# Optimization experiments

Hardware: AMD Instinct MI355X
Metric: run time of the kernel (lower is better)

Reference implementation:

```python
import jax, jax.numpy as jnp
import numpy as np

B, S, D = 2, 2048, 1024
H = 16
HD = D // H
MINUS_INFINITY = -1000000000.0


def setup_inputs() -> dict:
    key = jax.random.key(0)
    ks = jax.random.split(key, 6)
    sc = 0.02
    return {
        "x": jax.random.normal(ks[0], (B, S, D), dtype=jnp.float32),
        "Wq": jax.random.normal(ks[1], (D, D), dtype=jnp.float32) * sc,
        "Wk": jax.random.normal(ks[2], (D, D), dtype=jnp.float32) * sc,
        "Wv": jax.random.normal(ks[3], (D, D), dtype=jnp.float32) * sc,
        "Wo": jax.random.normal(ks[4], (D, D), dtype=jnp.float32) * sc,
        "bo": jnp.zeros((D,), dtype=jnp.float32),
    }


def reference(x, Wq, Wk, Wv, Wo, bo):
    b, n, _ = x.shape
    # Linear with transpose_b=True: x @ W.T
    q = jnp.einsum('bnd,ed->bne', x, Wq).reshape(b, n, H, HD).transpose(0, 2, 1, 3)
    k = jnp.einsum('bnd,ed->bne', x, Wk).reshape(b, n, H, HD).transpose(0, 2, 1, 3)
    v = jnp.einsum('bnd,ed->bne', x, Wv).reshape(b, n, H, HD).transpose(0, 2, 1, 3)
    scores = jnp.einsum('bhqd,bhkd->bhqk', q, k) * (1.0 / HD ** 0.5)
    mask = jnp.triu(jnp.ones((n, n), dtype=scores.dtype), k=1) * MINUS_INFINITY
    scores = scores + mask[None, None, :, :]
    attn = jax.nn.softmax(scores, axis=-1)  # dropout prob = 0.0
    ctx = jnp.einsum('bhqk,bhkd->bhqd', attn, v)
    ctx = ctx.transpose(0, 2, 1, 3).reshape(b, n, D)
    return jnp.einsum('bnd,ed->bne', ctx, Wo) + bo
```

## Files before the change

### kernel.cpp

```cpp
#include <hip/hip_runtime.h>
#include <hip/hip_bf16.h>

#define B_  2
#define S_  2048
#define D_  1024
#define H_  16
#define HD_ 64

typedef __attribute__((ext_vector_type(8))) short short8;
typedef __attribute__((ext_vector_type(4))) float f32x4;

__device__ __forceinline__ unsigned short f2b(float f) {
    __hip_bfloat16 h = __float2bfloat16(f);
    unsigned short u;
    __builtin_memcpy(&u, &h, 2);
    return u;
}

typedef __attribute__((address_space(1))) const unsigned int g_u32;
typedef __attribute__((address_space(3))) unsigned int l_u32;
__device__ __forceinline__ void gload_lds16(const void* g, void* l) {
    __builtin_amdgcn_global_load_lds((g_u32*)g, (l_u32*)l, 16, 0, 0);
}

__global__ __launch_bounds__(256) void convert_kernel(
    const float* __restrict__ x,  const float* __restrict__ Wq,
    const float* __restrict__ Wk, const float* __restrict__ Wv,
    const float* __restrict__ Wo, unsigned short* __restrict__ dst)
{
    const long long i4 = blockIdx.x * 256 + threadIdx.x;
    const long long e  = i4 * 4;
    const long long M1 = 1048576LL;
    const float* src;
    if      (e < 4 * M1) src = x  + e;
    else if (e < 5 * M1) src = Wq + (e - 4 * M1);
    else if (e < 6 * M1) src = Wk + (e - 5 * M1);
    else if (e < 7 * M1) src = Wv + (e - 6 * M1);
    else                 src = Wo + (e - 7 * M1);
    float4 v = *(const float4*)src;
    unsigned long long pk = (unsigned long long)f2b(v.x)
                          | ((unsigned long long)f2b(v.y) << 16)
                          | ((unsigned long long)f2b(v.z) << 32)
                          | ((unsigned long long)f2b(v.w) << 48);
    *(unsigned long long*)&dst[e] = pk;
}

__global__ __launch_bounds__(256) void qkv_proj_kernel(
    const unsigned short* __restrict__ x,
    const unsigned short* __restrict__ Wq,
    const unsigned short* __restrict__ Wk,
    const unsigned short* __restrict__ Wv,
    unsigned short* __restrict__ q_ws,
    unsigned short* __restrict__ k_ws,
    unsigned short* __restrict__ vT_ws)
{
    __shared__ unsigned short a_lds[128 * 64];
    __shared__ unsigned short b_lds[128 * 64];

    const int m0 = blockIdx.x * 128;
    const int n0 = blockIdx.y * 128;
    const int which = blockIdx.z;
    const unsigned short* W = (which == 0) ? Wq : (which == 1) ? Wk : Wv;

    const int tid  = threadIdx.x;
    const int wave = tid >> 6;
    const int lane = tid & 63;
    const int l15  = lane & 15;
    const int quad = lane >> 4;
    const int wm = (wave & 1) * 64;
    const int wn = (wave >> 1) * 64;
    const int xr = (l15 & 7) << 3;

    f32x4 acc[4][4];
    #pragma unroll
    for (int sm = 0; sm < 4; ++sm)
        #pragma unroll
        for (int sn = 0; sn < 4; ++sn)
            #pragma unroll
            for (int r = 0; r < 4; ++r) acc[sm][sn][r] = 0.f;

    for (int kk = 0; kk < D_; kk += 64) {
        #pragma unroll
        for (int p = 0; p < 4; ++p) {
            const int off = (p * 256 + tid) * 16;
            const int r   = off >> 7;
            const int cs  = ((off & 127) >> 1) ^ ((r & 7) << 3);
            gload_lds16(&x[(m0 + r) * D_ + kk + cs], &a_lds[off >> 1]);
            gload_lds16(&W[(n0 + r) * D_ + kk + cs], &b_lds[off >> 1]);
        }
        __syncthreads();
        #pragma unroll
        for (int kc = 0; kc < 2; ++kc) {
            const int cswz = (kc * 32 + quad * 8) ^ xr;
            short8 af[4], bf[4];
            #pragma unroll
            for (int s = 0; s < 4; ++s) {
                af[s] = *(const short8*)&a_lds[(wm + s * 16 + l15) * 64 + cswz];
                bf[s] = *(const short8*)&b_lds[(wn + s * 16 + l15) * 64 + cswz];
            }
            #pragma unroll
            for (int sm = 0; sm < 4; ++sm)
                #pragma unroll
                for (int sn = 0; sn < 4; ++sn)
                    acc[sm][sn] = __builtin_amdgcn_mfma_f32_16x16x32_bf16(
                        af[sm], bf[sn], acc[sm][sn], 0, 0, 0);
        }
        __syncthreads();
    }

    #pragma unroll
    for (int sm = 0; sm < 4; ++sm) {
        #pragma unroll
        for (int sn = 0; sn < 4; ++sn) {
            const int n  = n0 + wn + sn * 16 + l15;
            const int h  = n >> 6;
            const int hd = n & 63;
            const int mbase = m0 + wm + sm * 16 + quad * 4;
            const int b     = mbase >> 11;
            const int sbase = mbase & 2047;
            if (which == 2) {
                unsigned long long pk = 0;
                #pragma unroll
                for (int r = 0; r < 4; ++r)
                    pk |= (unsigned long long)f2b(acc[sm][sn][r]) << (16 * r);
                *(unsigned long long*)&vT_ws[((b * H_ + h) * HD_ + hd) * S_ + sbase] = pk;
            } else if (which == 0) {
                #pragma unroll
                for (int r = 0; r < 4; ++r)
                    q_ws[((b * H_ + h) * S_ + (sbase + r)) * HD_ + hd] =
                        f2b(acc[sm][sn][r] * 0.125f);
            } else {
                #pragma unroll
                for (int r = 0; r < 4; ++r)
                    k_ws[((b * H_ + h) * S_ + (sbase + r)) * HD_ + hd] =
                        f2b(acc[sm][sn][r]);
            }
        }
    }
}

__global__ __launch_bounds__(256) void attn_kernel(
    const unsigned short* __restrict__ q_ws,
    const unsigned short* __restrict__ k_ws,
    const unsigned short* __restrict__ vT_ws,
    unsigned short* __restrict__ ctx_ws)
{
    __shared__ unsigned short k_lds[2][64][72];
    __shared__ unsigned short vT_lds[2][64][72];

    const int bh = blockIdx.x;
    const int qt = 31 - (int)blockIdx.y;

    const int tid  = threadIdx.x;
    const int wave = tid >> 6;
    const int lane = tid & 63;
    const int l15  = lane & 15;
    const int quad = lane >> 4;
    const int row  = tid >> 3;
    const int c8   = tid & 7;

    const unsigned short* Qh = q_ws + bh * (S_ * HD_);
    const unsigned short* Kh = k_ws + bh * (S_ * HD_);
    const unsigned short* Vt = vT_ws + bh * (HD_ * S_);
    const int b = bh >> 4;
    const int h = bh & 15;

    const int src0 = l15 + 32 * (quad & 1);
    const int src1 = src0 + 16;
    const int sel  = quad >> 1;

    const int q0 = qt * 64;
    const int qg = q0 + wave * 16 + l15;

    *(uint4*)&k_lds[0][row][c8 * 8]       = *(const uint4*)&Kh[row * HD_ + c8 * 8];
    *(uint4*)&k_lds[0][row + 32][c8 * 8]  = *(const uint4*)&Kh[(row + 32) * HD_ + c8 * 8];
    *(uint4*)&vT_lds[0][row][c8 * 8]      = *(const uint4*)&Vt[row * S_ + c8 * 8];
    *(uint4*)&vT_lds[0][row + 32][c8 * 8] = *(const uint4*)&Vt[(row + 32) * S_ + c8 * 8];

    short8 aq[2];
    aq[0] = *(const short8*)&Qh[qg * HD_ + quad * 8];
    aq[1] = *(const short8*)&Qh[qg * HD_ + 32 + quad * 8];

    __syncthreads();

    float l_lane = 0.f;
    f32x4 o[4];
    #pragma unroll
    for (int f = 0; f < 4; ++f)
        #pragma unroll
        for (int r = 0; r < 4; ++r) o[f][r] = 0.f;

    for (int kt = 0; kt <= qt; ++kt) {
        const int cur = kt & 1;
        if (kt < qt) {
            const int nk0 = (kt + 1) * 64;
            const int nb  = cur ^ 1;
            *(uint4*)&k_lds[nb][row][c8 * 8]       = *(const uint4*)&Kh[(nk0 + row) * HD_ + c8 * 8];
            *(uint4*)&k_lds[nb][row + 32][c8 * 8]  = *(const uint4*)&Kh[(nk0 + row + 32) * HD_ + c8 * 8];
            *(uint4*)&vT_lds[nb][row][c8 * 8]      = *(const uint4*)&Vt[row * S_ + nk0 + c8 * 8];
            *(uint4*)&vT_lds[nb][row + 32][c8 * 8] = *(const uint4*)&Vt[(row + 32) * S_ + nk0 + c8 * 8];
        }

        f32x4 sc[4];
        #pragma unroll
        for (int f = 0; f < 4; ++f)
            #pragma unroll
            for (int r = 0; r < 4; ++r) sc[f][r] = 0.f;
        #pragma unroll
        for (int f = 0; f < 4; ++f)
            #pragma unroll
            for (int kc = 0; kc < 2; ++kc) {
                short8 ak = *(const short8*)&k_lds[cur][f * 16 + l15][kc * 32 + quad * 8];
                sc[f] = __builtin_amdgcn_mfma_f32_16x16x32_bf16(ak, aq[kc], sc[f], 0, 0, 0);
            }

        float p[4][4];
        if (kt == qt) {
            const int kbase = kt * 64 + quad * 4;
            #pragma unroll
            for (int f = 0; f < 4; ++f)
                #pragma unroll
                for (int r = 0; r < 4; ++r) {
                    const float pv = __expf(sc[f][r]);
                    p[f][r] = (kbase + f * 16 + r > qg) ? 0.f : pv;
                    l_lane += p[f][r];
                }
        } else {
            #pragma unroll
            for (int f = 0; f < 4; ++f)
                #pragma unroll
                for (int r = 0; r < 4; ++r) {
                    p[f][r] = __expf(sc[f][r]);
                    l_lane += p[f][r];
                }
        }

        unsigned int pd[4][2];
        #pragma unroll
        for (int f = 0; f < 4; ++f) {
            pd[f][0] = (unsigned int)f2b(p[f][0]) | ((unsigned int)f2b(p[f][1]) << 16);
            pd[f][1] = (unsigned int)f2b(p[f][2]) | ((unsigned int)f2b(p[f][3]) << 16);
        }

        #pragma unroll
        for (int c = 0; c < 2; ++c) {
            const int a0 = __shfl((int)pd[c * 2][0],     src0, 64);
            const int a1 = __shfl((int)pd[c * 2][1],     src0, 64);
            const int a2 = __shfl((int)pd[c * 2][0],     src1, 64);
            const int a3 = __shfl((int)pd[c * 2][1],     src1, 64);
            const int b0 = __shfl((int)pd[c * 2 + 1][0], src0, 64);
            const int b1 = __shfl((int)pd[c * 2 + 1][1], src0, 64);
            const int b2 = __shfl((int)pd[c * 2 + 1][0], src1, 64);
            const int b3 = __shfl((int)pd[c * 2 + 1][1], src1, 64);
            union { int i[4]; short8 s; } u2;
            u2.i[0] = sel ? b0 : a0;
            u2.i[1] = sel ? b1 : a1;
            u2.i[2] = sel ? b2 : a2;
            u2.i[3] = sel ? b3 : a3;
            #pragma unroll
            for (int f = 0; f < 4; ++f) {
                short8 av = *(const short8*)&vT_lds[cur][f * 16 + l15][c * 32 + quad * 8];
                o[f] = __builtin_amdgcn_mfma_f32_16x16x32_bf16(av, u2.s, o[f], 0, 0, 0);
            }
        }

        __syncthreads();
    }

    float l = l_lane;
    l += __shfl_xor(l, 16, 64);
    l += __shfl_xor(l, 32, 64);
    const float inv_l = 1.0f / l;

    #pragma unroll
    for (int f = 0; f < 4; ++f) {
        unsigned long long pk = 0;
        #pragma unroll
        for (int r = 0; r < 4; ++r)
            pk |= (unsigned long long)f2b(o[f][r] * inv_l) << (16 * r);
        *(unsigned long long*)&ctx_ws[(b * S_ + qg) * D_ + h * 64 + f * 16 + quad * 4] = pk;
    }
}

__global__ __launch_bounds__(256) void out_proj_kernel(
    const unsigned short* __restrict__ ctx,
    const unsigned short* __restrict__ Wo,
    const float* __restrict__ bo,
    float* __restrict__ out)
{
    __shared__ unsigned short a_lds[128 * 64];
    __shared__ unsigned short b_lds[128 * 64];

    const int m0 = blockIdx.x * 128;
    const int n0 = blockIdx.y * 128;

    const int tid  = threadIdx.x;
    const int wave = tid >> 6;
    const int lane = tid & 63;
    const int l15  = lane & 15;
    const int quad = lane >> 4;
    const int wm = (wave & 1) * 64;
    const int wn = (wave >> 1) * 64;
    const int xr = (l15 & 7) << 3;

    f32x4 acc[4][4];
    #pragma unroll
    for (int sm = 0; sm < 4; ++sm)
        #pragma unroll
        for (int sn = 0; sn < 4; ++sn)
            #pragma unroll
            for (int r = 0; r < 4; ++r) acc[sm][sn][r] = 0.f;

    for (int kk = 0; kk < D_; kk += 64) {
        #pragma unroll
        for (int p = 0; p < 4; ++p) {
            const int off = (p * 256 + tid) * 16;
            const int r   = off >> 7;
            const int cs  = ((off & 127) >> 1) ^ ((r & 7) << 3);
            gload_lds16(&ctx[(m0 + r) * D_ + kk + cs], &a_lds[off >> 1]);
            gload_lds16(&Wo[(n0 + r) * D_ + kk + cs],  &b_lds[off >> 1]);
        }
        __syncthreads();
        #pragma unroll
        for (int kc = 0; kc < 2; ++kc) {
            const int cswz = (kc * 32 + quad * 8) ^ xr;
            short8 af[4], bf[4];
            #pragma unroll
            for (int s = 0; s < 4; ++s) {
                af[s] = *(const short8*)&a_lds[(wm + s * 16 + l15) * 64 + cswz];
                bf[s] = *(const short8*)&b_lds[(wn + s * 16 + l15) * 64 + cswz];
            }
            #pragma unroll
            for (int sm = 0; sm < 4; ++sm)
                #pragma unroll
                for (int sn = 0; sn < 4; ++sn)
                    acc[sm][sn] = __builtin_amdgcn_mfma_f32_16x16x32_bf16(
                        af[sm], bf[sn], acc[sm][sn], 0, 0, 0);
        }
        __syncthreads();
    }

    #pragma unroll
    for (int sm = 0; sm < 4; ++sm) {
        #pragma unroll
        for (int sn = 0; sn < 4; ++sn) {
            const int n = n0 + wn + sn * 16 + l15;
            const float bias = bo[n];
            const int mbase = m0 + wm + sm * 16 + quad * 4;
            #pragma unroll
            for (int r = 0; r < 4; ++r)
                out[(mbase + r) * D_ + n] = acc[sm][sn][r] + bias;
        }
    }
}

extern "C" void kernel_launch(void* const* d_in, const int* in_sizes, int n_in,
                              void* d_out, int out_size, void* d_ws, size_t ws_size,
                              hipStream_t stream) {
    const float* x  = (const float*)d_in[0];
    const float* Wq = (const float*)d_in[1];
    const float* Wk = (const float*)d_in[2];
    const float* Wv = (const float*)d_in[3];
    const float* Wo = (const float*)d_in[4];
    const float* bo = (const float*)d_in[5];
    float* out = (float*)d_out;

    const size_t M1 = 1048576;
    const size_t SZ = 4 * M1;

    unsigned short* xb  = (unsigned short*)d_ws;
    unsigned short* wqb = xb  + SZ;
    unsigned short* wkb = wqb + M1;
    unsigned short* wvb = wkb + M1;
    unsigned short* wob = wvb + M1;
    unsigned short* q_ws   = wob + M1;
    unsigned short* k_ws   = q_ws + SZ;
    unsigned short* vT_ws  = k_ws + SZ;
    unsigned short* ctx_ws = vT_ws + SZ;

    convert_kernel<<<dim3(8192), 256, 0, stream>>>(x, Wq, Wk, Wv, Wo, xb);
    qkv_proj_kernel<<<dim3(32, 8, 3), 256, 0, stream>>>(xb, wqb, wkb, wvb, q_ws, k_ws, vT_ws);
    attn_kernel<<<dim3(32, 32), 256, 0, stream>>>(q_ws, k_ws, vT_ws, ctx_ws);
    out_proj_kernel<<<dim3(32, 8), 256, 0, stream>>>(ctx_ws, wob, bo, out);
}
```

Measured before the change: 182.1 us.

## Load attention K/V tiles directly to LDS with XOR swizzle and exp2 softmax

The attention kernel now stages K and V^T tiles with global_load_lds (direct global-to-LDS) instead of going through registers. It replaces the padded LDS layout with an unpadded one that uses an XOR swizzle to avoid bank conflicts. Q is pre-scaled by log2(e) so the softmax can use exp2 instead of exp, and s_setprio raises wave priority around the MFMA blocks. This is meant to cut register traffic and VALU work in the inner loop. The direct LDS loads depend on the existing barrier for correctness with double buffering.

Result: no change. 185.4 us (+1.8%).

```diff
diff --git a/kernel.cpp b/kernel.cpp
--- a/kernel.cpp
+++ b/kernel.cpp
@@ -128,7 +128,7 @@
                 #pragma unroll
                 for (int r = 0; r < 4; ++r)
                     q_ws[((b * H_ + h) * S_ + (sbase + r)) * HD_ + hd] =
-                        f2b(acc[sm][sn][r] * 0.125f);
+                        f2b(acc[sm][sn][r] * (0.125f * 1.44269504f));
             } else {
                 #pragma unroll
                 for (int r = 0; r < 4; ++r)
@@ -145,8 +145,8 @@
     const unsigned short* __restrict__ vT_ws,
     unsigned short* __restrict__ ctx_ws)
 {
-    __shared__ unsigned short k_lds[2][64][72];
-    __shared__ unsigned short vT_lds[2][64][72];
+    __shared__ unsigned short k_lds[2 * 64 * 64];
+    __shared__ unsigned short vT_lds[2 * 64 * 64];
 
     const int bh = blockIdx.x;
     const int qt = 31 - (int)blockIdx.y;
@@ -156,7 +156,7 @@
     const int lane = tid & 63;
     const int l15  = lane & 15;
     const int quad = lane >> 4;
-    const int row  = tid >> 3;
+    const int r0   = tid >> 3;
     const int c8   = tid & 7;
 
     const unsigned short* Qh = q_ws + bh * (S_ * HD_);
@@ -169,13 +169,17 @@
     const int src1 = src0 + 16;
     const int sel  = quad >> 1;
 
-    const int q0 = qt * 64;
-    const int qg = q0 + wave * 16 + l15;
-
-    *(uint4*)&k_lds[0][row][c8 * 8]       = *(const uint4*)&Kh[row * HD_ + c8 * 8];
-    *(uint4*)&k_lds[0][row + 32][c8 * 8]  = *(const uint4*)&Kh[(row + 32) * HD_ + c8 * 8];
-    *(uint4*)&vT_lds[0][row][c8 * 8]      = *(const uint4*)&Vt[row * S_ + c8 * 8];
-    *(uint4*)&vT_lds[0][row + 32][c8 * 8] = *(const uint4*)&Vt[(row + 32) * S_ + c8 * 8];
+    const int qg = qt * 64 + wave * 16 + l15;
+
+    const int scol = (c8 ^ (r0 & 7)) * 8;
+    const int d0 = r0 * 64 + c8 * 8;
+    const int d1 = d0 + 2048;
+    const int xr8 = (l15 & 7) << 3;
+
+    gload_lds16(&Kh[r0 * HD_ + scol],        &k_lds[d0]);
+    gload_lds16(&Kh[(r0 + 32) * HD_ + scol], &k_lds[d1]);
+    gload_lds16(&Vt[r0 * S_ + scol],         &vT_lds[d0]);
+    gload_lds16(&Vt[(r0 + 32) * S_ + scol],  &vT_lds[d1]);
 
     short8 aq[2];
     aq[0] = *(const short8*)&Qh[qg * HD_ + quad * 8];
@@ -191,14 +195,14 @@
         for (int r = 0; r < 4; ++r) o[f][r] = 0.f;
 
     for (int kt = 0; kt <= qt; ++kt) {
-        const int cur = kt & 1;
+        const int cb = (kt & 1) * 4096;
         if (kt < qt) {
             const int nk0 = (kt + 1) * 64;
-            const int nb  = cur ^ 1;
-            *(uint4*)&k_lds[nb][row][c8 * 8]       = *(const uint4*)&Kh[(nk0 + row) * HD_ + c8 * 8];
-            *(uint4*)&k_lds[nb][row + 32][c8 * 8]  = *(const uint4*)&Kh[(nk0 + row + 32) * HD_ + c8 * 8];
-            *(uint4*)&vT_lds[nb][row][c8 * 8]      = *(const uint4*)&Vt[row * S_ + nk0 + c8 * 8];
-            *(uint4*)&vT_lds[nb][row + 32][c8 * 8] = *(const uint4*)&Vt[(row + 32) * S_ + nk0 + c8 * 8];
+            const int nbb = 4096 - cb;
+            gload_lds16(&Kh[(nk0 + r0) * HD_ + scol],      &k_lds[nbb + d0]);
+            gload_lds16(&Kh[(nk0 + r0 + 32) * HD_ + scol], &k_lds[nbb + d1]);
+            gload_lds16(&Vt[r0 * S_ + nk0 + scol],         &vT_lds[nbb + d0]);
+            gload_lds16(&Vt[(r0 + 32) * S_ + nk0 + scol],  &vT_lds[nbb + d1]);
         }
 
         f32x4 sc[4];
@@ -206,13 +210,16 @@
         for (int f = 0; f < 4; ++f)
             #pragma unroll
             for (int r = 0; r < 4; ++r) sc[f][r] = 0.f;
+        __builtin_amdgcn_s_setprio(1);
         #pragma unroll
         for (int f = 0; f < 4; ++f)
             #pragma unroll
             for (int kc = 0; kc < 2; ++kc) {
-                short8 ak = *(const short8*)&k_lds[cur][f * 16 + l15][kc * 32 + quad * 8];
+                short8 ak = *(const short8*)&k_lds[cb + (f * 16 + l15) * 64
+                                                  + ((kc * 32 + quad * 8) ^ xr8)];
                 sc[f] = __builtin_amdgcn_mfma_f32_16x16x32_bf16(ak, aq[kc], sc[f], 0, 0, 0);
             }
+        __builtin_amdgcn_s_setprio(0);
 
         float p[4][4];
         if (kt == qt) {
@@ -221,7 +228,7 @@
             for (int f = 0; f < 4; ++f)
                 #pragma unroll
                 for (int r = 0; r < 4; ++r) {
-                    const float pv = __expf(sc[f][r]);
+                    const float pv = __builtin_exp2f(sc[f][r]);
                     p[f][r] = (kbase + f * 16 + r > qg) ? 0.f : pv;
                     l_lane += p[f][r];
                 }
@@ -230,7 +237,7 @@
             for (int f = 0; f < 4; ++f)
                 #pragma unroll
                 for (int r = 0; r < 4; ++r) {
-                    p[f][r] = __expf(sc[f][r]);
+                    p[f][r] = __builtin_exp2f(sc[f][r]);
                     l_lane += p[f][r];
                 }
         }
@@ -257,11 +264,14 @@
             u2.i[1] = sel ? b1 : a1;
             u2.i[2] = sel ? b2 : a2;
             u2.i[3] = sel ? b3 : a3;
+            __builtin_amdgcn_s_setprio(1);
             #pragma unroll
             for (int f = 0; f < 4; ++f) {
-                short8 av = *(const short8*)&vT_lds[cur][f * 16 + l15][c * 32 + quad * 8];
+                short8 av = *(const short8*)&vT_lds[cb + (f * 16 + l15) * 64
+                                                   + ((c * 32 + quad * 8) ^ xr8)];
                 o[f] = __builtin_amdgcn_mfma_f32_16x16x32_bf16(av, u2.s, o[f], 0, 0, 0);
             }
+            __builtin_amdgcn_s_setprio(0);
         }
 
         __syncthreads();
```
